# Kernel optimization log

Hardware: AMD Instinct MI355X
Metric: run time of the kernel (lower is better)

Reference implementation:

```python
import jax, jax.numpy as jnp
import numpy as np

D_MODEL = 384
KSIZE = 3
B, L = 32, 512
LN_EPS = 1e-5


def _conv1d_same(x, w, b):
    # x: [B, C_in, L], w: [C_out, C_in, K] -> [B, C_out, L]
    y = jax.lax.conv_general_dilated(
        x, w, window_strides=(1,), padding='SAME',
        dimension_numbers=('NCH', 'OIH', 'NCH'))
    return y + b[None, :, None]


def _conv_fft_block(x, wa, ba, wb, bb):
    # Conv1D_FFT: transpose -> conv/relu -> conv/relu -> transpose back
    h = jnp.transpose(x, (0, 2, 1))            # [B, D, L]
    h = jax.nn.relu(_conv1d_same(h, wa, ba))
    h = jax.nn.relu(_conv1d_same(h, wb, bb))
    return jnp.transpose(h, (0, 2, 1))         # [B, L, D]


def _layernorm(x, g, b):
    mu = jnp.mean(x, axis=-1, keepdims=True)
    var = jnp.var(x, axis=-1, keepdims=True)
    return (x - mu) * jax.lax.rsqrt(var + LN_EPS) * g + b


def setup_inputs() -> dict:
    key = jax.random.key(0)
    ks = jax.random.split(key, 8)
    x = jax.random.normal(ks[0], (B, L, D_MODEL), dtype=jnp.float32)
    durations = jax.random.randint(ks[1], (B, L), 0, 8, dtype=jnp.int32)
    s = 0.02
    params = {
        'c1a_w': jax.random.normal(ks[2], (D_MODEL, D_MODEL, KSIZE), jnp.float32) * s,
        'c1a_b': jnp.zeros((D_MODEL,), jnp.float32),
        'c1b_w': jax.random.normal(ks[3], (D_MODEL, D_MODEL, KSIZE), jnp.float32) * s,
        'c1b_b': jnp.zeros((D_MODEL,), jnp.float32),
        'ln1_g': jnp.ones((D_MODEL,), jnp.float32),
        'ln1_b': jnp.zeros((D_MODEL,), jnp.float32),
        'c2a_w': jax.random.normal(ks[4], (D_MODEL, D_MODEL, KSIZE), jnp.float32) * s,
        'c2a_b': jnp.zeros((D_MODEL,), jnp.float32),
        'c2b_w': jax.random.normal(ks[5], (D_MODEL, D_MODEL, KSIZE), jnp.float32) * s,
        'c2b_b': jnp.zeros((D_MODEL,), jnp.float32),
        'ln2_g': jnp.ones((D_MODEL,), jnp.float32),
        'ln2_b': jnp.zeros((D_MODEL,), jnp.float32),
        'lin_w': jax.random.normal(ks[6], (D_MODEL, 1), jnp.float32) * s,
        'lin_b': jnp.zeros((1,), jnp.float32),
    }
    return {'x': x, 'durations': durations, **params}


def reference(x, durations, c1a_w, c1a_b, c1b_w, c1b_b, ln1_g, ln1_b,
              c2a_w, c2a_b, c2b_w, c2b_b, ln2_g, ln2_b, lin_w, lin_b):
    # --- DurationPredictor (dropout = identity, eval mode) ---
    h = _conv_fft_block(x, c1a_w, c1a_b, c1b_w, c1b_b)
    h = _layernorm(h, ln1_g, ln1_b)
    h = _conv_fft_block(h, c2a_w, c2a_b, c2b_w, c2b_b)
    h = _layernorm(h, ln2_g, ln2_b)
    dur_preds = (h @ lin_w + lin_b)[..., 0]      # [B, L]

    # --- LR: duration-based expansion via one-hot alignment matmul ---
    total = jnp.sum(durations, axis=-1)          # [B]
    T = int(jnp.max(total))                      # concrete (durations are input data)
    cum = jnp.cumsum(durations, axis=-1)         # [B, L]
    t = jnp.arange(T, dtype=cum.dtype)           # [T]
    # frame t belongs to phoneme j s.t. cum[j-1] <= t < cum[j]
    idx = jax.vmap(lambda c: jnp.searchsorted(c, t, side='right'))(cum)  # [B, T]
    mask = (t[None, :] < total[:, None]).astype(x.dtype)                 # [B, T]
    align = jax.nn.one_hot(idx, x.shape[1], dtype=x.dtype) * mask[:, :, None]  # [B, T, L]
    out = jnp.einsum('btl,bld->btd', align, x)   # [B, T, D]
    return (out, dur_preds)
```

## Files before the change

### kernel.cpp

```cpp
#include <hip/hip_runtime.h>

#define B_   32
#define L_   512
#define D_   384
#define M_   (B_*L_)
#define KTOT (D_*3)
#define LDW  392
#define BROWS 82
#define BUFE (BROWS*LDW)

typedef __bf16 bf16x8 __attribute__((ext_vector_type(8)));
typedef float  floatx4 __attribute__((ext_vector_type(4)));

__global__ __launch_bounds__(256) void repack4_kernel(const float* __restrict__ wa,
                                                      const float* __restrict__ wb,
                                                      const float* __restrict__ wc,
                                                      const float* __restrict__ wd,
                                                      __bf16* __restrict__ oa,
                                                      __bf16* __restrict__ ob,
                                                      __bf16* __restrict__ oc,
                                                      __bf16* __restrict__ od)
{
    int idx = blockIdx.x * 256 + threadIdx.x;
    if (idx >= D_ * KTOT) return;
    const float* w; __bf16* o_;
    switch (blockIdx.y) {
        case 0:  w = wa; o_ = oa; break;
        case 1:  w = wb; o_ = ob; break;
        case 2:  w = wc; o_ = oc; break;
        default: w = wd; o_ = od; break;
    }
    int j  = idx & 7;
    int l  = (idx >> 3) & 63;
    int ct = idx >> 9;
    int c  = ct / 24;
    int t  = ct - c * 24;
    int o  = t * 16 + (l & 15);
    int kflat = c * 32 + (l >> 4) * 8 + j;
    int s  = kflat / D_;
    int i  = kflat - s * D_;
    o_[idx] = (__bf16)w[(o * D_ + i) * 3 + s];
}

__global__ __launch_bounds__(512, 1) void fused_predictor(
    const float* __restrict__ x,
    const __bf16* __restrict__ w1a, const float* __restrict__ b1a,
    const __bf16* __restrict__ w1b, const float* __restrict__ b1b,
    const float* __restrict__ g1,  const float* __restrict__ e1,
    const __bf16* __restrict__ w2a, const float* __restrict__ b2a,
    const __bf16* __restrict__ w2b, const float* __restrict__ b2b,
    const float* __restrict__ g2,  const float* __restrict__ e2,
    const float* __restrict__ lw,  const float* __restrict__ lb,
    float* __restrict__ out_dur)
{
    extern __shared__ char smem_raw[];
    __bf16* bufA = (__bf16*)smem_raw;
    __bf16* bufB = bufA + BUFE;
    float*  red1 = (float*)(bufB + BUFE);
    float*  red2 = red1 + BROWS * 8;
    float*  minv = red2 + BROWS * 8;

    const int m0 = blockIdx.x * 64;
    const int l0 = m0 & 511;
    const int b0 = m0 - l0;

    const int tid  = threadIdx.x;
    const int wave = tid >> 6;
    const int lane = tid & 63;
    const int quad = lane >> 4;
    const int lx   = lane & 15;

    bf16x8 kz;
#pragma unroll
    for (int z = 0; z < 8; z++) kz[z] = (__bf16)0.f;

    for (int c = tid; c < BROWS * 48; c += 512) {
        int beta = c / 48, q = c - beta * 48;
        int l = l0 + beta - 9;
        bf16x8 v = kz;
        if ((unsigned)l < (unsigned)L_) {
            const float* xr = x + (size_t)(b0 + l) * D_ + q * 8;
            const float4 f0 = *(const float4*)xr;
            const float4 f1 = *(const float4*)(xr + 4);
            v[0] = (__bf16)f0.x; v[1] = (__bf16)f0.y; v[2] = (__bf16)f0.z; v[3] = (__bf16)f0.w;
            v[4] = (__bf16)f1.x; v[5] = (__bf16)f1.y; v[6] = (__bf16)f1.z; v[7] = (__bf16)f1.w;
        }
        *(bf16x8*)(&bufA[beta * LDW + q * 8]) = v;
    }
    for (int c = tid; c < 2 * 48; c += 512) {
        int beta = (c < 48) ? 0 : 81, q = c % 48;
        *(bf16x8*)(&bufB[beta * LDW + q * 8]) = kz;
    }
    __syncthreads();

    const int t0  = wave * 3;
    const int col0 = wave * 48 + lx;

    floatx4 acc[5][3];
    bf16x8  bg[3][3];

    for (int st = 0; st < 4; st++) {
        const __bf16* bin  = (st & 1) ? bufB : bufA;
        __bf16*       bout = (st & 1) ? bufA : bufB;
        const __bf16* Wp = (st == 0) ? w1a : (st == 1) ? w1b : (st == 2) ? w2a : w2b;
        const float*  bp = (st == 0) ? b1a : (st == 1) ? b1b : (st == 2) ? b2a : b2b;

#pragma unroll
        for (int mt = 0; mt < 5; mt++)
#pragma unroll
            for (int ni = 0; ni < 3; ni++)
#pragma unroll
                for (int r = 0; r < 4; r++) acc[mt][ni][r] = 0.f;

        const char* pb0 = (const char*)Wp + ((size_t)t0 * 64 + lane) * 16;
        auto loadB = [&](int buf, int n) {
            int it = n / 3, s = n - it * 3;
            const char* p = pb0 + (size_t)(s * 12 + it) * 24576;
#pragma unroll
            for (int ni = 0; ni < 3; ni++)
                bg[buf][ni] = *(const bf16x8*)(p + ni * 1024);
        };
        loadB(0, 0); loadB(1, 1);

        const __bf16* ab = bin + lx * LDW + quad * 8;
#pragma unroll
        for (int n = 0; n < 36; n++) {
            const int it = n / 3, s = n - it * 3;
            if (n + 2 < 36) loadB((n + 2) % 3, n + 2);
            bf16x8 af[5];
#pragma unroll
            for (int mt = 0; mt < 5; mt++)
                af[mt] = *(const bf16x8*)(ab + (mt * 16 + s) * LDW + it * 32);
#pragma unroll
            for (int mt = 0; mt < 5; mt++)
#pragma unroll
                for (int ni = 0; ni < 3; ni++)
                    acc[mt][ni] = __builtin_amdgcn_mfma_f32_16x16x32_bf16(af[mt], bg[n % 3][ni], acc[mt][ni], 0, 0, 0);
        }

        float bv[3];
#pragma unroll
        for (int ni = 0; ni < 3; ni++) bv[ni] = bp[col0 + ni * 16];
#pragma unroll
        for (int mt = 0; mt < 5; mt++)
#pragma unroll
            for (int ni = 0; ni < 3; ni++)
#pragma unroll
                for (int r = 0; r < 4; r++) {
                    float vv = acc[mt][ni][r] + bv[ni];
                    acc[mt][ni][r] = vv > 0.f ? vv : 0.f;
                }

        if (st == 1 || st == 3) {
#pragma unroll
            for (int mt = 0; mt < 5; mt++)
#pragma unroll
                for (int r = 0; r < 4; r++) {
                    float s1 = acc[mt][0][r] + acc[mt][1][r] + acc[mt][2][r];
                    float s2 = acc[mt][0][r] * acc[mt][0][r] + acc[mt][1][r] * acc[mt][1][r]
                             + acc[mt][2][r] * acc[mt][2][r];
#pragma unroll
                    for (int d = 1; d < 16; d <<= 1) {
                        s1 += __shfl_xor(s1, d);
                        s2 += __shfl_xor(s2, d);
                    }
                    if (lx == 0) {
                        int beta = mt * 16 + quad * 4 + r + 1;
                        red1[beta * 8 + wave] = s1;
                        red2[beta * 8 + wave] = s2;
                    }
                }
            __syncthreads();
            if (tid < BROWS) {
                float s1 = 0.f, s2 = 0.f;
#pragma unroll
                for (int w = 0; w < 8; w++) { s1 += red1[tid * 8 + w]; s2 += red2[tid * 8 + w]; }
                float mean = s1 * (1.f / D_);
                float var  = s2 * (1.f / D_) - mean * mean;
                minv[tid * 2]     = mean;
                minv[tid * 2 + 1] = rsqrtf(var + 1e-5f);
            }
            __syncthreads();
            const float* gp = (st == 1) ? g1 : g2;
            const float* ep = (st == 1) ? e1 : e2;
            float gv[3], ev[3];
#pragma unroll
            for (int ni = 0; ni < 3; ni++) { gv[ni] = gp[col0 + ni * 16]; ev[ni] = ep[col0 + ni * 16]; }
#pragma unroll
            for (int mt = 0; mt < 5; mt++)
#pragma unroll
                for (int r = 0; r < 4; r++) {
                    int beta = mt * 16 + quad * 4 + r + 1;
                    float mean = minv[beta * 2], inv = minv[beta * 2 + 1];
#pragma unroll
                    for (int ni = 0; ni < 3; ni++)
                        acc[mt][ni][r] = (acc[mt][ni][r] - mean) * inv * gv[ni] + ev[ni];
                }
            if (st == 1) {
#pragma unroll
                for (int mt = 0; mt < 5; mt++)
#pragma unroll
                    for (int r = 0; r < 4; r++) {
                        int beta = mt * 16 + quad * 4 + r + 1;
                        bool ok = (unsigned)(l0 + beta - 9) < (unsigned)L_;
#pragma unroll
                        for (int ni = 0; ni < 3; ni++)
                            bout[beta * LDW + col0 + ni * 16] = (__bf16)(ok ? acc[mt][ni][r] : 0.f);
                    }
            } else {
                float lwv[3];
#pragma unroll
                for (int ni = 0; ni < 3; ni++) lwv[ni] = lw[col0 + ni * 16];
#pragma unroll
                for (int mt = 0; mt < 5; mt++)
#pragma unroll
                    for (int r = 0; r < 4; r++) {
                        float p = acc[mt][0][r] * lwv[0] + acc[mt][1][r] * lwv[1] + acc[mt][2][r] * lwv[2];
#pragma unroll
                        for (int d = 1; d < 16; d <<= 1) p += __shfl_xor(p, d);
                        if (lx == 0) {
                            int beta = mt * 16 + quad * 4 + r + 1;
                            red1[beta * 8 + wave] = p;
                        }
                    }
                __syncthreads();
                if (tid < 64) {
                    int beta = tid + 9;
                    float sacc = lb[0];
#pragma unroll
                    for (int w = 0; w < 8; w++) sacc += red1[beta * 8 + w];
                    out_dur[m0 + tid] = sacc;
                }
            }
        } else {
#pragma unroll
            for (int mt = 0; mt < 5; mt++)
#pragma unroll
                for (int r = 0; r < 4; r++) {
                    int beta = mt * 16 + quad * 4 + r + 1;
                    bool ok = (unsigned)(l0 + beta - 9) < (unsigned)L_;
#pragma unroll
                    for (int ni = 0; ni < 3; ni++)
                        bout[beta * LDW + col0 + ni * 16] = (__bf16)(ok ? acc[mt][ni][r] : 0.f);
                }
        }
        __syncthreads();
    }
}

__global__ __launch_bounds__(64) void cum_kernel(const int* __restrict__ dur,
                                                 int* __restrict__ cum)
{
    int b = blockIdx.x, lane = threadIdx.x;
    const int* db = dur + b * L_;
    int v[8], s = 0;
#pragma unroll
    for (int i = 0; i < 8; i++) { v[i] = db[lane * 8 + i]; s += v[i]; }
    int ex = s;
#pragma unroll
    for (int off = 1; off < 64; off <<= 1) {
        int n = __shfl_up(ex, off);
        if (lane >= off) ex += n;
    }
    ex -= s;
    int c = ex;
    int* cb = cum + b * L_;
#pragma unroll
    for (int i = 0; i < 8; i++) { c += v[i]; cb[lane * 8 + i] = c; }
}

__global__ __launch_bounds__(128) void gather_kernel(const float* __restrict__ x,
                                                     const int* __restrict__ cum,
                                                     float* __restrict__ out, int T)
{
    int fr = blockIdx.x;
    int b  = fr / T;
    int t  = fr - b * T;
    int tid = threadIdx.x;
    const int* cb = cum + b * L_;
    int total = cb[L_ - 1];
    float4 val = make_float4(0.f, 0.f, 0.f, 0.f);
    if (t < total) {
        int lo = 0, hi = L_;
        while (lo < hi) { int mid = (lo + hi) >> 1; if (cb[mid] > t) hi = mid; else lo = mid + 1; }
        if (tid < 96) val = *(const float4*)(x + ((size_t)(b * L_ + lo)) * D_ + tid * 4);
    }
    if (tid < 96) *(float4*)(out + (size_t)fr * D_ + tid * 4) = val;
}

extern "C" void kernel_launch(void* const* d_in, const int* in_sizes, int n_in,
                              void* d_out, int out_size, void* d_ws, size_t ws_size,
                              hipStream_t stream) {
    const float* x       = (const float*)d_in[0];
    const int*   dur     = (const int*)d_in[1];
    const float* c1a_w   = (const float*)d_in[2];
    const float* c1a_b   = (const float*)d_in[3];
    const float* c1b_w   = (const float*)d_in[4];
    const float* c1b_b   = (const float*)d_in[5];
    const float* ln1_g   = (const float*)d_in[6];
    const float* ln1_b   = (const float*)d_in[7];
    const float* c2a_w   = (const float*)d_in[8];
    const float* c2a_b   = (const float*)d_in[9];
    const float* c2b_w   = (const float*)d_in[10];
    const float* c2b_b   = (const float*)d_in[11];
    const float* ln2_g   = (const float*)d_in[12];
    const float* ln2_b   = (const float*)d_in[13];
    const float* lin_w   = (const float*)d_in[14];
    const float* lin_b   = (const float*)d_in[15];

    const int T = (out_size - B_ * L_) / (B_ * D_);
    float* out_gather = (float*)d_out;
    float* out_dur    = (float*)d_out + (size_t)B_ * T * D_;

    char* p = (char*)d_ws;
    __bf16* w1a = (__bf16*)p; p += (size_t)D_ * KTOT * 2;
    __bf16* w1b = (__bf16*)p; p += (size_t)D_ * KTOT * 2;
    __bf16* w2a = (__bf16*)p; p += (size_t)D_ * KTOT * 2;
    __bf16* w2b = (__bf16*)p; p += (size_t)D_ * KTOT * 2;
    int* cum = (int*)p; p += (size_t)B_ * L_ * 4;

    cum_kernel<<<B_, 64, 0, stream>>>(dur, cum);
    gather_kernel<<<B_ * T, 128, 0, stream>>>(x, cum, out_gather, T);

    dim3 rpgrid((D_ * KTOT + 255) / 256, 4);
    repack4_kernel<<<rpgrid, 256, 0, stream>>>(c1a_w, c1b_w, c2a_w, c2b_w, w1a, w1b, w2a, w2b);

    const size_t smem = (size_t)2 * BUFE * 2 + (BROWS * 8 * 2 + BROWS * 2) * 4;
    static bool attr_set = false;
    if (!attr_set) {
        hipFuncSetAttribute((const void*)fused_predictor,
                            hipFuncAttributeMaxDynamicSharedMemorySize, (int)smem);
        attr_set = true;
    }
    fused_predictor<<<256, 512, smem, stream>>>(
        x, w1a, c1a_b, w1b, c1b_b, ln1_g, ln1_b,
        w2a, c2a_b, w2b, c2b_b, ln2_g, ln2_b,
        lin_w, lin_b, out_dur);
}
```

Baseline: 255.0 us.

## Retile fused conv stack as 2x4 wave grid with wider N per wave

Each wave previously computed all 5 M-tiles by 48 columns. Waves are now arranged as 2 M-groups by 4 N-groups, each covering 96 columns and either 3 or 2 M-tiles. This halves the per-wave weight fetches relative to the output computed and cuts LDS A-fragment reads, and the LayerNorm and linear reductions now sum over 4 partials instead of 8. The MFMA loop is also wrapped in s_setprio to favour matrix issue. In exchange, register use rises (18 accumulators plus triple-buffered 6-wide B fragments) and the M split is uneven, so one group of waves idles on 2-tile work.

```diff
diff --git a/kernel.cpp b/kernel.cpp
--- a/kernel.cpp
+++ b/kernel.cpp
@@ -69,6 +69,10 @@
     const int lane = tid & 63;
     const int quad = lane >> 4;
     const int lx   = lane & 15;
+    const int ng   = wave & 3;
+    const int mg   = wave >> 2;
+    const int mtc  = mg ? 2 : 3;
+    const int mtb  = mg ? 3 : 0;
 
     bf16x8 kz;
 #pragma unroll
@@ -93,11 +97,11 @@
     }
     __syncthreads();
 
-    const int t0  = wave * 3;
-    const int col0 = wave * 48 + lx;
-
-    floatx4 acc[5][3];
-    bf16x8  bg[3][3];
+    const int t0   = ng * 6;
+    const int col0 = ng * 96 + lx;
+
+    floatx4 acc[3][6];
+    bf16x8  bg[3][6];
 
     for (int st = 0; st < 4; st++) {
         const __bf16* bin  = (st & 1) ? bufB : bufA;
@@ -106,75 +110,91 @@
         const float*  bp = (st == 0) ? b1a : (st == 1) ? b1b : (st == 2) ? b2a : b2b;
 
 #pragma unroll
-        for (int mt = 0; mt < 5; mt++)
-#pragma unroll
-            for (int ni = 0; ni < 3; ni++)
-#pragma unroll
-                for (int r = 0; r < 4; r++) acc[mt][ni][r] = 0.f;
+        for (int mt = 0; mt < 3; mt++)
+            if (mt < mtc)
+#pragma unroll
+                for (int ni = 0; ni < 6; ni++)
+#pragma unroll
+                    for (int r = 0; r < 4; r++) acc[mt][ni][r] = 0.f;
 
         const char* pb0 = (const char*)Wp + ((size_t)t0 * 64 + lane) * 16;
         auto loadB = [&](int buf, int n) {
             int it = n / 3, s = n - it * 3;
             const char* p = pb0 + (size_t)(s * 12 + it) * 24576;
 #pragma unroll
-            for (int ni = 0; ni < 3; ni++)
+            for (int ni = 0; ni < 6; ni++)
                 bg[buf][ni] = *(const bf16x8*)(p + ni * 1024);
         };
         loadB(0, 0); loadB(1, 1);
 
-        const __bf16* ab = bin + lx * LDW + quad * 8;
+        const __bf16* ab = bin + (mtb * 16 + lx) * LDW + quad * 8;
 #pragma unroll
         for (int n = 0; n < 36; n++) {
             const int it = n / 3, s = n - it * 3;
             if (n + 2 < 36) loadB((n + 2) % 3, n + 2);
-            bf16x8 af[5];
-#pragma unroll
-            for (int mt = 0; mt < 5; mt++)
-                af[mt] = *(const bf16x8*)(ab + (mt * 16 + s) * LDW + it * 32);
-#pragma unroll
-            for (int mt = 0; mt < 5; mt++)
-#pragma unroll
-                for (int ni = 0; ni < 3; ni++)
-                    acc[mt][ni] = __builtin_amdgcn_mfma_f32_16x16x32_bf16(af[mt], bg[n % 3][ni], acc[mt][ni], 0, 0, 0);
+            bf16x8 af[3];
+            af[0] = *(const bf16x8*)(ab + (s) * LDW + it * 32);
+            af[1] = *(const bf16x8*)(ab + (16 + s) * LDW + it * 32);
+            if (mtc == 3)
+                af[2] = *(const bf16x8*)(ab + (32 + s) * LDW + it * 32);
+            __builtin_amdgcn_s_setprio(1);
+#pragma unroll
+            for (int ni = 0; ni < 6; ni++) {
+                acc[0][ni] = __builtin_amdgcn_mfma_f32_16x16x32_bf16(af[0], bg[n % 3][ni], acc[0][ni], 0, 0, 0);
+                acc[1][ni] = __builtin_amdgcn_mfma_f32_16x16x32_bf16(af[1], bg[n % 3][ni], acc[1][ni], 0, 0, 0);
+            }
+            if (mtc == 3) {
+#pragma unroll
+                for (int ni = 0; ni < 6; ni++)
+                    acc[2][ni] = __builtin_amdgcn_mfma_f32_16x16x32_bf16(af[2], bg[n % 3][ni], acc[2][ni], 0, 0, 0);
+            }
+            __builtin_amdgcn_s_setprio(0);
         }
 
-        float bv[3];
-#pragma unroll
-        for (int ni = 0; ni < 3; ni++) bv[ni] = bp[col0 + ni * 16];
-#pragma unroll
-        for (int mt = 0; mt < 5; mt++)
-#pragma unroll
-            for (int ni = 0; ni < 3; ni++)
-#pragma unroll
-                for (int r = 0; r < 4; r++) {
-                    float vv = acc[mt][ni][r] + bv[ni];
-                    acc[mt][ni][r] = vv > 0.f ? vv : 0.f;
-                }
+        float bv[6];
+#pragma unroll
+        for (int ni = 0; ni < 6; ni++) bv[ni] = bp[col0 + ni * 16];
+#pragma unroll
+        for (int mt = 0; mt < 3; mt++)
+            if (mt < mtc)
+#pragma unroll
+                for (int ni = 0; ni < 6; ni++)
+#pragma unroll
+                    for (int r = 0; r < 4; r++) {
+                        float vv = acc[mt][ni][r] + bv[ni];
+                        acc[mt][ni][r] = vv > 0.f ? vv : 0.f;
+                    }
 
         if (st == 1 || st == 3) {
 #pragma unroll
-            for (int mt = 0; mt < 5; mt++)
-#pragma unroll
-                for (int r = 0; r < 4; r++) {
-                    float s1 = acc[mt][0][r] + acc[mt][1][r] + acc[mt][2][r];
-                    float s2 = acc[mt][0][r] * acc[mt][0][r] + acc[mt][1][r] * acc[mt][1][r]
-                             + acc[mt][2][r] * acc[mt][2][r];
-#pragma unroll
-                    for (int d = 1; d < 16; d <<= 1) {
-                        s1 += __shfl_xor(s1, d);
-                        s2 += __shfl_xor(s2, d);
+            for (int mt = 0; mt < 3; mt++)
+                if (mt < mtc)
+#pragma unroll
+                    for (int r = 0; r < 4; r++) {
+                        float s1 = 0.f, s2 = 0.f;
+#pragma unroll
+                        for (int ni = 0; ni < 6; ni++) {
+                            s1 += acc[mt][ni][r];
+                            s2 += acc[mt][ni][r] * acc[mt][ni][r];
+                        }
+#pragma unroll
+                        for (int d = 1; d < 16; d <<= 1) {
+                            s1 += __shfl_xor(s1, d);
+                            s2 += __shfl_xor(s2, d);
+                        }
+                        if (lx == 0) {
+                            int beta = (mtb + mt) * 16 + quad * 4 + r + 1;
+                            red1[beta * 8 + wave] = s1;
+                            red2[beta * 8 + wave] = s2;
+                        }
                     }
-                    if (lx == 0) {
-                        int beta = mt * 16 + quad * 4 + r + 1;
-                        red1[beta * 8 + wave] = s1;
-                        red2[beta * 8 + wave] = s2;
-                    }
-                }
             __syncthreads();
             if (tid < BROWS) {
+                int tile = (tid - 1) >> 4;
+                int base = (tile >= 3) ? 4 : 0;
                 float s1 = 0.f, s2 = 0.f;
 #pragma unroll
-                for (int w = 0; w < 8; w++) { s1 += red1[tid * 8 + w]; s2 += red2[tid * 8 + w]; }
+                for (int k = 0; k < 4; k++) { s1 += red1[tid * 8 + base + k]; s2 += red2[tid * 8 + base + k]; }
                 float mean = s1 * (1.f / D_);
                 float var  = s2 * (1.f / D_) - mean * mean;
                 minv[tid * 2]     = mean;
@@ -183,66 +203,74 @@
             __syncthreads();
             const float* gp = (st == 1) ? g1 : g2;
             const float* ep = (st == 1) ? e1 : e2;
-            float gv[3], ev[3];
-#pragma unroll
-            for (int ni = 0; ni < 3; ni++) { gv[ni] = gp[col0 + ni * 16]; ev[ni] = ep[col0 + ni * 16]; }
-#pragma unroll
-            for (int mt = 0; mt < 5; mt++)
-#pragma unroll
-                for (int r = 0; r < 4; r++) {
-                    int beta = mt * 16 + quad * 4 + r + 1;
-                    float mean = minv[beta * 2], inv = minv[beta * 2 + 1];
-#pragma unroll
-                    for (int ni = 0; ni < 3; ni++)
-                        acc[mt][ni][r] = (acc[mt][ni][r] - mean) * inv * gv[ni] + ev[ni];
-                }
+            float gv[6], ev[6];
+#pragma unroll
+            for (int ni = 0; ni < 6; ni++) { gv[ni] = gp[col0 + ni * 16]; ev[ni] = ep[col0 + ni * 16]; }
+#pragma unroll
+            for (int mt = 0; mt < 3; mt++)
+                if (mt < mtc)
+#pragma unroll
+                    for (int r = 0; r < 4; r++) {
+                        int beta = (mtb + mt) * 16 + quad * 4 + r + 1;
+                        float mean = minv[beta * 2], inv = minv[beta * 2 + 1];
+#pragma unroll
+                        for (int ni = 0; ni < 6; ni++)
+                            acc[mt][ni][r] = (acc[mt][ni][r] - mean) * inv * gv[ni] + ev[ni];
+                    }
             if (st == 1) {
 #pragma unroll
-                for (int mt = 0; mt < 5; mt++)
-#pragma unroll
-                    for (int r = 0; r < 4; r++) {
-                        int beta = mt * 16 + quad * 4 + r + 1;
-                        bool ok = (unsigned)(l0 + beta - 9) < (unsigned)L_;
-#pragma unroll
-                        for (int ni = 0; ni < 3; ni++)
-                            bout[beta * LDW + col0 + ni * 16] = (__bf16)(ok ? acc[mt][ni][r] : 0.f);
-                    }
+                for (int mt = 0; mt < 3; mt++)
+                    if (mt < mtc)
+#pragma unroll
+                        for (int r = 0; r < 4; r++) {
+                            int beta = (mtb + mt) * 16 + quad * 4 + r + 1;
+                            bool ok = (unsigned)(l0 + beta - 9) < (unsigned)L_;
+#pragma unroll
+                            for (int ni = 0; ni < 6; ni++)
+                                bout[beta * LDW + col0 + ni * 16] = (__bf16)(ok ? acc[mt][ni][r] : 0.f);
+                        }
             } else {
-                float lwv[3];
-#pragma unroll
-                for (int ni = 0; ni < 3; ni++) lwv[ni] = lw[col0 + ni * 16];
-#pragma unroll
-                for (int mt = 0; mt < 5; mt++)
-#pragma unroll
-                    for (int r = 0; r < 4; r++) {
-                        float p = acc[mt][0][r] * lwv[0] + acc[mt][1][r] * lwv[1] + acc[mt][2][r] * lwv[2];
-#pragma unroll
-                        for (int d = 1; d < 16; d <<= 1) p += __shfl_xor(p, d);
-                        if (lx == 0) {
-                            int beta = mt * 16 + quad * 4 + r + 1;
-                            red1[beta * 8 + wave] = p;
-                        }
-                    }
+                float lwv[6];
+#pragma unroll
+                for (int ni = 0; ni < 6; ni++) lwv[ni] = lw[col0 + ni * 16];
+#pragma unroll
+                for (int mt = 0; mt < 3; mt++)
+                    if (mt < mtc)
+#pragma unroll
+                        for (int r = 0; r < 4; r++) {
+                            float p = 0.f;
+#pragma unroll
+                            for (int ni = 0; ni < 6; ni++) p += acc[mt][ni][r] * lwv[ni];
+#pragma unroll
+                            for (int d = 1; d < 16; d <<= 1) p += __shfl_xor(p, d);
+                            if (lx == 0) {
+                                int beta = (mtb + mt) * 16 + quad * 4 + r + 1;
+                                red1[beta * 8 + wave] = p;
+                            }
+                        }
                 __syncthreads();
                 if (tid < 64) {
                     int beta = tid + 9;
+                    int tile = (beta - 1) >> 4;
+                    int base = (tile >= 3) ? 4 : 0;
                     float sacc = lb[0];
 #pragma unroll
-                    for (int w = 0; w < 8; w++) sacc += red1[beta * 8 + w];
+                    for (int k = 0; k < 4; k++) sacc += red1[beta * 8 + base + k];
                     out_dur[m0 + tid] = sacc;
                 }
             }
         } else {
 #pragma unroll
-            for (int mt = 0; mt < 5; mt++)
-#pragma unroll
-                for (int r = 0; r < 4; r++) {
-                    int beta = mt * 16 + quad * 4 + r + 1;
-                    bool ok = (unsigned)(l0 + beta - 9) < (unsigned)L_;
-#pragma unroll
-                    for (int ni = 0; ni < 3; ni++)
-                        bout[beta * LDW + col0 + ni * 16] = (__bf16)(ok ? acc[mt][ni][r] : 0.f);
-                }
+            for (int mt = 0; mt < 3; mt++)
+                if (mt < mtc)
+#pragma unroll
+                    for (int r = 0; r < 4; r++) {
+                        int beta = (mtb + mt) * 16 + quad * 4 + r + 1;
+                        bool ok = (unsigned)(l0 + beta - 9) < (unsigned)L_;
+#pragma unroll
+                        for (int ni = 0; ni < 6; ni++)
+                            bout[beta * LDW + col0 + ni * 16] = (__bf16)(ok ? acc[mt][ni][r] : 0.f);
+                    }
         }
         __syncthreads();
     }
```

Result: no change. 251.9 us (-1.2%).

## Halve predictor row tile, use single in-place LDS buffer, raise MFMA priority

Applied to the files above, without the earlier changes.

Each block of the fused predictor now handles 32 sequence rows instead of 64, computing 48 rows including the halo, so the grid doubles to 512 blocks. The two ping-pong LDS buffers are replaced by one buffer updated in place, with an extra barrier before each write-back. The MFMA section is wrapped in s_setprio. The aim is to cut LDS use and registers enough that more blocks or waves can share a CU and hide latency. The cost is a larger halo-recompute fraction, twice the total weight reads across blocks, and an additional barrier per stage.

```diff
diff --git a/kernel.cpp b/kernel.cpp
--- a/kernel.cpp
+++ b/kernel.cpp
@@ -6,7 +6,7 @@
 #define M_   (B_*L_)
 #define KTOT (D_*3)
 #define LDW  392
-#define BROWS 82
+#define BROWS 50
 #define BUFE (BROWS*LDW)
 
 typedef __bf16 bf16x8 __attribute__((ext_vector_type(8)));
@@ -54,13 +54,12 @@
     float* __restrict__ out_dur)
 {
     extern __shared__ char smem_raw[];
-    __bf16* bufA = (__bf16*)smem_raw;
-    __bf16* bufB = bufA + BUFE;
-    float*  red1 = (float*)(bufB + BUFE);
+    __bf16* buf  = (__bf16*)smem_raw;
+    float*  red1 = (float*)(buf + BUFE);
     float*  red2 = red1 + BROWS * 8;
     float*  minv = red2 + BROWS * 8;
 
-    const int m0 = blockIdx.x * 64;
+    const int m0 = blockIdx.x * 32;
     const int l0 = m0 & 511;
     const int b0 = m0 - l0;
 
@@ -85,64 +84,61 @@
             v[0] = (__bf16)f0.x; v[1] = (__bf16)f0.y; v[2] = (__bf16)f0.z; v[3] = (__bf16)f0.w;
             v[4] = (__bf16)f1.x; v[5] = (__bf16)f1.y; v[6] = (__bf16)f1.z; v[7] = (__bf16)f1.w;
         }
-        *(bf16x8*)(&bufA[beta * LDW + q * 8]) = v;
-    }
-    for (int c = tid; c < 2 * 48; c += 512) {
-        int beta = (c < 48) ? 0 : 81, q = c % 48;
-        *(bf16x8*)(&bufB[beta * LDW + q * 8]) = kz;
+        *(bf16x8*)(&buf[beta * LDW + q * 8]) = v;
     }
     __syncthreads();
 
-    const int t0  = wave * 3;
+    const int t0   = wave * 3;
     const int col0 = wave * 48 + lx;
 
-    floatx4 acc[5][3];
+    floatx4 acc[3][3];
     bf16x8  bg[3][3];
 
     for (int st = 0; st < 4; st++) {
-        const __bf16* bin  = (st & 1) ? bufB : bufA;
-        __bf16*       bout = (st & 1) ? bufA : bufB;
         const __bf16* Wp = (st == 0) ? w1a : (st == 1) ? w1b : (st == 2) ? w2a : w2b;
         const float*  bp = (st == 0) ? b1a : (st == 1) ? b1b : (st == 2) ? b2a : b2b;
 
 #pragma unroll
-        for (int mt = 0; mt < 5; mt++)
+        for (int mt = 0; mt < 3; mt++)
 #pragma unroll
             for (int ni = 0; ni < 3; ni++)
 #pragma unroll
                 for (int r = 0; r < 4; r++) acc[mt][ni][r] = 0.f;
 
         const char* pb0 = (const char*)Wp + ((size_t)t0 * 64 + lane) * 16;
-        auto loadB = [&](int buf, int n) {
+        auto loadB = [&](int bufi, int n) {
             int it = n / 3, s = n - it * 3;
             const char* p = pb0 + (size_t)(s * 12 + it) * 24576;
 #pragma unroll
             for (int ni = 0; ni < 3; ni++)
-                bg[buf][ni] = *(const bf16x8*)(p + ni * 1024);
+                bg[bufi][ni] = *(const bf16x8*)(p + ni * 1024);
         };
         loadB(0, 0); loadB(1, 1);
 
-        const __bf16* ab = bin + lx * LDW + quad * 8;
+        const __bf16* ab = buf + lx * LDW + quad * 8;
 #pragma unroll
         for (int n = 0; n < 36; n++) {
             const int it = n / 3, s = n - it * 3;
             if (n + 2 < 36) loadB((n + 2) % 3, n + 2);
-            bf16x8 af[5];
-#pragma unroll
-            for (int mt = 0; mt < 5; mt++)
-                af[mt] = *(const bf16x8*)(ab + (mt * 16 + s) * LDW + it * 32);
-#pragma unroll
-            for (int mt = 0; mt < 5; mt++)
-#pragma unroll
-                for (int ni = 0; ni < 3; ni++)
-                    acc[mt][ni] = __builtin_amdgcn_mfma_f32_16x16x32_bf16(af[mt], bg[n % 3][ni], acc[mt][ni], 0, 0, 0);
+            bf16x8 af[3];
+            af[0] = *(const bf16x8*)(ab + (s) * LDW + it * 32);
+            af[1] = *(const bf16x8*)(ab + (16 + s) * LDW + it * 32);
+            af[2] = *(const bf16x8*)(ab + (32 + s) * LDW + it * 32);
+            __builtin_amdgcn_s_setprio(1);
+#pragma unroll
+            for (int ni = 0; ni < 3; ni++) {
+                acc[0][ni] = __builtin_amdgcn_mfma_f32_16x16x32_bf16(af[0], bg[n % 3][ni], acc[0][ni], 0, 0, 0);
+                acc[1][ni] = __builtin_amdgcn_mfma_f32_16x16x32_bf16(af[1], bg[n % 3][ni], acc[1][ni], 0, 0, 0);
+                acc[2][ni] = __builtin_amdgcn_mfma_f32_16x16x32_bf16(af[2], bg[n % 3][ni], acc[2][ni], 0, 0, 0);
+            }
+            __builtin_amdgcn_s_setprio(0);
         }
 
         float bv[3];
 #pragma unroll
         for (int ni = 0; ni < 3; ni++) bv[ni] = bp[col0 + ni * 16];
 #pragma unroll
-        for (int mt = 0; mt < 5; mt++)
+        for (int mt = 0; mt < 3; mt++)
 #pragma unroll
             for (int ni = 0; ni < 3; ni++)
 #pragma unroll
@@ -153,12 +149,15 @@
 
         if (st == 1 || st == 3) {
 #pragma unroll
-            for (int mt = 0; mt < 5; mt++)
+            for (int mt = 0; mt < 3; mt++)
 #pragma unroll
                 for (int r = 0; r < 4; r++) {
-                    float s1 = acc[mt][0][r] + acc[mt][1][r] + acc[mt][2][r];
-                    float s2 = acc[mt][0][r] * acc[mt][0][r] + acc[mt][1][r] * acc[mt][1][r]
-                             + acc[mt][2][r] * acc[mt][2][r];
+                    float s1 = 0.f, s2 = 0.f;
+#pragma unroll
+                    for (int ni = 0; ni < 3; ni++) {
+                        s1 += acc[mt][ni][r];
+                        s2 += acc[mt][ni][r] * acc[mt][ni][r];
+                    }
 #pragma unroll
                     for (int d = 1; d < 16; d <<= 1) {
                         s1 += __shfl_xor(s1, d);
@@ -174,7 +173,7 @@
             if (tid < BROWS) {
                 float s1 = 0.f, s2 = 0.f;
 #pragma unroll
-                for (int w = 0; w < 8; w++) { s1 += red1[tid * 8 + w]; s2 += red2[tid * 8 + w]; }
+                for (int k = 0; k < 8; k++) { s1 += red1[tid * 8 + k]; s2 += red2[tid * 8 + k]; }
                 float mean = s1 * (1.f / D_);
                 float var  = s2 * (1.f / D_) - mean * mean;
                 minv[tid * 2]     = mean;
@@ -187,7 +186,7 @@
 #pragma unroll
             for (int ni = 0; ni < 3; ni++) { gv[ni] = gp[col0 + ni * 16]; ev[ni] = ep[col0 + ni * 16]; }
 #pragma unroll
-            for (int mt = 0; mt < 5; mt++)
+            for (int mt = 0; mt < 3; mt++)
 #pragma unroll
                 for (int r = 0; r < 4; r++) {
                     int beta = mt * 16 + quad * 4 + r + 1;
@@ -198,24 +197,26 @@
                 }
             if (st == 1) {
 #pragma unroll
-                for (int mt = 0; mt < 5; mt++)
+                for (int mt = 0; mt < 3; mt++)
 #pragma unroll
                     for (int r = 0; r < 4; r++) {
                         int beta = mt * 16 + quad * 4 + r + 1;
                         bool ok = (unsigned)(l0 + beta - 9) < (unsigned)L_;
 #pragma unroll
                         for (int ni = 0; ni < 3; ni++)
-                            bout[beta * LDW + col0 + ni * 16] = (__bf16)(ok ? acc[mt][ni][r] : 0.f);
+                            buf[beta * LDW + col0 + ni * 16] = (__bf16)(ok ? acc[mt][ni][r] : 0.f);
                     }
             } else {
                 float lwv[3];
 #pragma unroll
                 for (int ni = 0; ni < 3; ni++) lwv[ni] = lw[col0 + ni * 16];
 #pragma unroll
-                for (int mt = 0; mt < 5; mt++)
+                for (int mt = 0; mt < 3; mt++)
 #pragma unroll
                     for (int r = 0; r < 4; r++) {
-                        float p = acc[mt][0][r] * lwv[0] + acc[mt][1][r] * lwv[1] + acc[mt][2][r] * lwv[2];
+                        float p = 0.f;
+#pragma unroll
+                        for (int ni = 0; ni < 3; ni++) p += acc[mt][ni][r] * lwv[ni];
 #pragma unroll
                         for (int d = 1; d < 16; d <<= 1) p += __shfl_xor(p, d);
                         if (lx == 0) {
@@ -224,24 +225,25 @@
                         }
                     }
                 __syncthreads();
-                if (tid < 64) {
+                if (tid < 32) {
                     int beta = tid + 9;
                     float sacc = lb[0];
 #pragma unroll
-                    for (int w = 0; w < 8; w++) sacc += red1[beta * 8 + w];
+                    for (int k = 0; k < 8; k++) sacc += red1[beta * 8 + k];
                     out_dur[m0 + tid] = sacc;
                 }
             }
         } else {
-#pragma unroll
-            for (int mt = 0; mt < 5; mt++)
+            __syncthreads();
+#pragma unroll
+            for (int mt = 0; mt < 3; mt++)
 #pragma unroll
                 for (int r = 0; r < 4; r++) {
                     int beta = mt * 16 + quad * 4 + r + 1;
                     bool ok = (unsigned)(l0 + beta - 9) < (unsigned)L_;
 #pragma unroll
                     for (int ni = 0; ni < 3; ni++)
-                        bout[beta * LDW + col0 + ni * 16] = (__bf16)(ok ? acc[mt][ni][r] : 0.f);
+                        buf[beta * LDW + col0 + ni * 16] = (__bf16)(ok ? acc[mt][ni][r] : 0.f);
                 }
         }
         __syncthreads();
@@ -325,14 +327,14 @@
     dim3 rpgrid((D_ * KTOT + 255) / 256, 4);
     repack4_kernel<<<rpgrid, 256, 0, stream>>>(c1a_w, c1b_w, c2a_w, c2b_w, w1a, w1b, w2a, w2b);
 
-    const size_t smem = (size_t)2 * BUFE * 2 + (BROWS * 8 * 2 + BROWS * 2) * 4;
+    const size_t smem = (size_t)BUFE * 2 + (BROWS * 8 * 2 + BROWS * 2) * 4;
     static bool attr_set = false;
     if (!attr_set) {
         hipFuncSetAttribute((const void*)fused_predictor,
                             hipFuncAttributeMaxDynamicSharedMemorySize, (int)smem);
         attr_set = true;
     }
-    fused_predictor<<<256, 512, smem, stream>>>(
+    fused_predictor<<<M_ / 32, 512, smem, stream>>>(
         x, w1a, c1a_b, w1b, c1b_b, ln1_g, ln1_b,
         w2a, c2a_b, w2b, c2b_b, ln2_g, ln2_b,
         lin_w, lin_b, out_dur);
```

Result: slower. 268.0 us (+5.1%).

## Stage conv weights cooperatively into triple-buffered LDS and reuse one activation buffer

Applied to the files above, without the earlier changes.

Before, each wave loaded its own weight fragments straight from global memory into registers with a prefetch. Now the whole block copies each weight K-chunk into a three-deep LDS ring and every wave reads its fragments from LDS, with a barrier after every K-step. The activation ping-pong buffers are merged into one buffer updated in place, and MFMA sections get raised wave priority. This is meant to overlap global weight fetches with compute and free LDS, but it adds 36 block barriers per stage plus extra LDS write and read traffic.

```diff
diff --git a/kernel.cpp b/kernel.cpp
--- a/kernel.cpp
+++ b/kernel.cpp
@@ -8,6 +8,7 @@
 #define LDW  392
 #define BROWS 82
 #define BUFE (BROWS*LDW)
+#define CHUNKE 12288
 
 typedef __bf16 bf16x8 __attribute__((ext_vector_type(8)));
 typedef float  floatx4 __attribute__((ext_vector_type(4)));
@@ -54,9 +55,9 @@
     float* __restrict__ out_dur)
 {
     extern __shared__ char smem_raw[];
-    __bf16* bufA = (__bf16*)smem_raw;
-    __bf16* bufB = bufA + BUFE;
-    float*  red1 = (float*)(bufB + BUFE);
+    __bf16* buf  = (__bf16*)smem_raw;
+    __bf16* cbs  = buf + BUFE;
+    float*  red1 = (float*)(cbs + 3 * CHUNKE);
     float*  red2 = red1 + BROWS * 8;
     float*  minv = red2 + BROWS * 8;
 
@@ -85,23 +86,15 @@
             v[0] = (__bf16)f0.x; v[1] = (__bf16)f0.y; v[2] = (__bf16)f0.z; v[3] = (__bf16)f0.w;
             v[4] = (__bf16)f1.x; v[5] = (__bf16)f1.y; v[6] = (__bf16)f1.z; v[7] = (__bf16)f1.w;
         }
-        *(bf16x8*)(&bufA[beta * LDW + q * 8]) = v;
-    }
-    for (int c = tid; c < 2 * 48; c += 512) {
-        int beta = (c < 48) ? 0 : 81, q = c % 48;
-        *(bf16x8*)(&bufB[beta * LDW + q * 8]) = kz;
-    }
-    __syncthreads();
-
-    const int t0  = wave * 3;
+        *(bf16x8*)(&buf[beta * LDW + q * 8]) = v;
+    }
+
+    const int t0   = wave * 3;
     const int col0 = wave * 48 + lx;
 
     floatx4 acc[5][3];
-    bf16x8  bg[3][3];
 
     for (int st = 0; st < 4; st++) {
-        const __bf16* bin  = (st & 1) ? bufB : bufA;
-        __bf16*       bout = (st & 1) ? bufA : bufB;
         const __bf16* Wp = (st == 0) ? w1a : (st == 1) ? w1b : (st == 2) ? w2a : w2b;
         const float*  bp = (st == 0) ? b1a : (st == 1) ? b1b : (st == 2) ? b2a : b2b;
 
@@ -112,30 +105,50 @@
 #pragma unroll
                 for (int r = 0; r < 4; r++) acc[mt][ni][r] = 0.f;
 
-        const char* pb0 = (const char*)Wp + ((size_t)t0 * 64 + lane) * 16;
-        auto loadB = [&](int buf, int n) {
-            int it = n / 3, s = n - it * 3;
-            const char* p = pb0 + (size_t)(s * 12 + it) * 24576;
-#pragma unroll
-            for (int ni = 0; ni < 3; ni++)
-                bg[buf][ni] = *(const bf16x8*)(p + ni * 1024);
-        };
-        loadB(0, 0); loadB(1, 1);
-
-        const __bf16* ab = bin + lx * LDW + quad * 8;
+        {
+            const bf16x8* s0 = (const bf16x8*)Wp + tid;
+            const bf16x8* s1 = (const bf16x8*)(Wp + 12 * CHUNKE) + tid;
+            bf16x8 a0 = s0[0], a1 = s0[512], a2 = s0[1024];
+            bf16x8 c0 = s1[0], c1 = s1[512], c2v = s1[1024];
+            bf16x8* d0 = (bf16x8*)cbs + tid;
+            bf16x8* d1 = (bf16x8*)(cbs + CHUNKE) + tid;
+            d0[0] = a0; d0[512] = a1; d0[1024] = a2;
+            d1[0] = c0; d1[512] = c1; d1[1024] = c2v;
+        }
+        __syncthreads();
+
+        const __bf16* ab = buf + lx * LDW + quad * 8;
 #pragma unroll
         for (int n = 0; n < 36; n++) {
             const int it = n / 3, s = n - it * 3;
-            if (n + 2 < 36) loadB((n + 2) % 3, n + 2);
+            bf16x8 sg0, sg1, sg2;
+            const bool do_stage = (n + 2 < 36);
+            if (do_stage) {
+                const int c2 = ((n + 2) % 3) * 12 + (n + 2) / 3;
+                const bf16x8* src = (const bf16x8*)(Wp + (size_t)c2 * CHUNKE) + tid;
+                sg0 = src[0]; sg1 = src[512]; sg2 = src[1024];
+            }
+            const __bf16* cbn = cbs + (n % 3) * CHUNKE;
+            bf16x8 bfr[3];
+#pragma unroll
+            for (int ni = 0; ni < 3; ni++)
+                bfr[ni] = *(const bf16x8*)(cbn + (t0 + ni) * 512 + lane * 8);
             bf16x8 af[5];
 #pragma unroll
             for (int mt = 0; mt < 5; mt++)
                 af[mt] = *(const bf16x8*)(ab + (mt * 16 + s) * LDW + it * 32);
+            __builtin_amdgcn_s_setprio(1);
 #pragma unroll
             for (int mt = 0; mt < 5; mt++)
 #pragma unroll
                 for (int ni = 0; ni < 3; ni++)
-                    acc[mt][ni] = __builtin_amdgcn_mfma_f32_16x16x32_bf16(af[mt], bg[n % 3][ni], acc[mt][ni], 0, 0, 0);
+                    acc[mt][ni] = __builtin_amdgcn_mfma_f32_16x16x32_bf16(af[mt], bfr[ni], acc[mt][ni], 0, 0, 0);
+            __builtin_amdgcn_s_setprio(0);
+            if (do_stage) {
+                bf16x8* d = (bf16x8*)(cbs + ((n + 2) % 3) * CHUNKE) + tid;
+                d[0] = sg0; d[512] = sg1; d[1024] = sg2;
+            }
+            __syncthreads();
         }
 
         float bv[3];
@@ -174,7 +187,7 @@
             if (tid < BROWS) {
                 float s1 = 0.f, s2 = 0.f;
 #pragma unroll
-                for (int w = 0; w < 8; w++) { s1 += red1[tid * 8 + w]; s2 += red2[tid * 8 + w]; }
+                for (int k = 0; k < 8; k++) { s1 += red1[tid * 8 + k]; s2 += red2[tid * 8 + k]; }
                 float mean = s1 * (1.f / D_);
                 float var  = s2 * (1.f / D_) - mean * mean;
                 minv[tid * 2]     = mean;
@@ -205,7 +218,7 @@
                         bool ok = (unsigned)(l0 + beta - 9) < (unsigned)L_;
 #pragma unroll
                         for (int ni = 0; ni < 3; ni++)
-                            bout[beta * LDW + col0 + ni * 16] = (__bf16)(ok ? acc[mt][ni][r] : 0.f);
+                            buf[beta * LDW + col0 + ni * 16] = (__bf16)(ok ? acc[mt][ni][r] : 0.f);
                     }
             } else {
                 float lwv[3];
@@ -228,7 +241,7 @@
                     int beta = tid + 9;
                     float sacc = lb[0];
 #pragma unroll
-                    for (int w = 0; w < 8; w++) sacc += red1[beta * 8 + w];
+                    for (int k = 0; k < 8; k++) sacc += red1[beta * 8 + k];
                     out_dur[m0 + tid] = sacc;
                 }
             }
@@ -241,10 +254,9 @@
                     bool ok = (unsigned)(l0 + beta - 9) < (unsigned)L_;
 #pragma unroll
                     for (int ni = 0; ni < 3; ni++)
-                        bout[beta * LDW + col0 + ni * 16] = (__bf16)(ok ? acc[mt][ni][r] : 0.f);
+                        buf[beta * LDW + col0 + ni * 16] = (__bf16)(ok ? acc[mt][ni][r] : 0.f);
                 }
         }
-        __syncthreads();
     }
 }
 
@@ -325,14 +337,14 @@
     dim3 rpgrid((D_ * KTOT + 255) / 256, 4);
     repack4_kernel<<<rpgrid, 256, 0, stream>>>(c1a_w, c1b_w, c2a_w, c2b_w, w1a, w1b, w2a, w2b);
 
-    const size_t smem = (size_t)2 * BUFE * 2 + (BROWS * 8 * 2 + BROWS * 2) * 4;
+    const size_t smem = (size_t)BUFE * 2 + 3 * 24576 + (BROWS * 8 * 2 + BROWS * 2) * 4;
     static bool attr_set = false;
     if (!attr_set) {
         hipFuncSetAttribute((const void*)fused_predictor,
                             hipFuncAttributeMaxDynamicSharedMemorySize, (int)smem);
         attr_set = true;
     }
-    fused_predictor<<<256, 512, smem, stream>>>(
+    fused_predictor<<<M_ / 64, 512, smem, stream>>>(
         x, w1a, c1a_b, w1b, c1b_b, ln1_g, ln1_b,
         w2a, c2a_b, w2b, c2b_b, ln2_g, ln2_b,
         lin_w, lin_b, out_dur);
```

Result: slower. 277.4 us (+8.8%).
